# Performance work log

Hardware: AMD Instinct MI355X
Metric: run time of the kernel (lower is better)

Reference implementation:

```python
import math
import jax, jax.numpy as jnp
import numpy as np

N_NODES = 100000
N_EDGES = 3200000
D = 128
H = 8
DK = D // H


def setup_inputs() -> dict:
    key = jax.random.key(0)
    ks = jax.random.split(key, 12)
    s = 1.0 / math.sqrt(D)
    return {
        "feat": jax.random.normal(ks[0], (N_NODES, D), jnp.float32),
        "Wk": jax.random.normal(ks[1], (D, D), jnp.float32) * s,
        "bk": jax.random.normal(ks[2], (D,), jnp.float32) * s,
        "Wq": jax.random.normal(ks[3], (D, D), jnp.float32) * s,
        "bq": jax.random.normal(ks[4], (D,), jnp.float32) * s,
        "Wv": jax.random.normal(ks[5], (D, D), jnp.float32) * s,
        "bv": jax.random.normal(ks[6], (D,), jnp.float32) * s,
        "w_att": jax.random.normal(ks[7], (H, DK, DK), jnp.float32) * (1.0 / math.sqrt(DK)),
        "w_msg": jax.random.normal(ks[8], (H, DK, DK), jnp.float32) * (1.0 / math.sqrt(DK)),
        "mu": jax.random.uniform(ks[9], (1,), jnp.float32, 0.5, 1.5),
        "src": jax.random.randint(ks[10], (N_EDGES,), 0, N_NODES, jnp.int32),
        "dst": jax.random.randint(ks[11], (N_EDGES,), 0, N_NODES, jnp.int32),
    }


def reference(feat, Wk, bk, Wq, bq, Wv, bv, w_att, w_msg, mu, src, dst):
    N = feat.shape[0]
    # node projections, per-head relation transforms
    k = (feat @ Wk.T + bk).reshape(N, H, DK)            # (N,H,dk)
    v = (feat @ Wv.T + bv).reshape(N, H, DK)
    q = (feat @ Wq.T + bq).reshape(N, H, DK)
    k = jnp.einsum('nhi,hij->nhj', k, w_att)
    v = jnp.einsum('nhi,hij->nhj', v, w_msg)
    # edge-wise q (dst) . k (src) attention logits
    logits = jnp.einsum('ehd,ehd->eh', q[dst], k[src])  # (E,H)
    logits = logits * (mu[0] / math.sqrt(DK))
    # segment softmax over incoming edges of each dst node
    m = jax.ops.segment_max(logits, dst, num_segments=N)   # (N,H)
    ex = jnp.exp(logits - m[dst])
    denom = jax.ops.segment_sum(ex, dst, num_segments=N)   # (N,H)
    attn = ex / denom[dst]                                  # (E,H)
    # weighted message aggregation
    msg = v[src] * attn[..., None]                          # (E,H,dk)
    h = jax.ops.segment_sum(msg, dst, num_segments=N)       # (N,H,dk)
    return h.reshape(N, H * DK)
```

## Files before the change

kernel.cpp:

```cpp
#include <hip/hip_runtime.h>
#include <hip/hip_bf16.h>
#include <hip/hip_fp16.h>
#include <stdint.h>

#define DD 128
#define HH 8
#define DKK 16

#define BSHIFT 7
#define BNODES (1 << BSHIFT)
#define SC_EPT 16

typedef __attribute__((ext_vector_type(8))) short bf16x8;
typedef __attribute__((ext_vector_type(4))) float f32x4;
typedef _Float16 h2 __attribute__((ext_vector_type(2)));
union u32h2 { unsigned u; h2 h; };

__device__ __forceinline__ float bfhi2f(unsigned u) {
  union { unsigned i; float f; } c; c.i = u & 0xFFFF0000u; return c.f;
}
__device__ __forceinline__ float bflo2f(unsigned u) {
  union { unsigned i; float f; } c; c.i = u << 16; return c.f;
}
__device__ __forceinline__ unsigned short f2bf(float f) {
  __hip_bfloat16 b = __float2bfloat16(f);
  return *reinterpret_cast<unsigned short*>(&b);
}

__global__ __launch_bounds__(256) void prep_weights(
    const float* __restrict__ Wq, const float* __restrict__ bq,
    const float* __restrict__ Wk, const float* __restrict__ bk,
    const float* __restrict__ Wv, const float* __restrict__ bv,
    const float* __restrict__ w_att, const float* __restrict__ w_msg,
    const float* __restrict__ mu,
    unsigned short* __restrict__ WcatT, float* __restrict__ bcat) {
  int gid = blockIdx.x * blockDim.x + threadIdx.x;
  if (gid >= DD * 384) return;
  int f = gid / 384;
  int o = gid % 384;
  float scale = mu[0] * 0.25f;
  float w;
  if (o < 128) {
    w = Wq[o * DD + f] * scale;
  } else if (o < 256) {
    int c = o - 128, h = c >> 4, j = c & 15;
    float s = 0.f;
#pragma unroll
    for (int i = 0; i < 16; ++i)
      s += Wk[(h * 16 + i) * DD + f] * w_att[h * 256 + i * 16 + j];
    w = s;
  } else {
    int c = o - 256, h = c >> 4, j = c & 15;
    float s = 0.f;
#pragma unroll
    for (int i = 0; i < 16; ++i)
      s += Wv[(h * 16 + i) * DD + f] * w_msg[h * 256 + i * 16 + j];
    w = s;
  }
  WcatT[(size_t)o * DD + f] = f2bf(w);
  if (f == 0) {
    float b;
    if (o < 128) {
      b = bq[o] * scale;
    } else if (o < 256) {
      int c = o - 128, h = c >> 4, j = c & 15;
      float s = 0.f;
#pragma unroll
      for (int i = 0; i < 16; ++i)
        s += bk[h * 16 + i] * w_att[h * 256 + i * 16 + j];
      b = s;
    } else {
      int c = o - 256, h = c >> 4, j = c & 15;
      float s = 0.f;
#pragma unroll
      for (int i = 0; i < 16; ++i)
        s += bv[h * 16 + i] * w_msg[h * 256 + i * 16 + j];
      b = s;
    }
    bcat[o] = b;
  }
}

__global__ __launch_bounds__(256) void proj_gemm(
    const float* __restrict__ feat, const unsigned short* __restrict__ WcatT,
    const float* __restrict__ bcat, float* __restrict__ Q,
    unsigned char* __restrict__ KVrow, unsigned short* __restrict__ S,
    int N) {
  int row0 = blockIdx.x * 128;
  int wave = threadIdx.x >> 6, lane = threadIdx.x & 63;
  int lrow = lane & 15, lk = lane >> 4;

  bf16x8 a0[4], a1[4];
#pragma unroll
  for (int fr = 0; fr < 2; ++fr) {
    int arow = row0 + wave * 32 + fr * 16 + lrow;
    const float* ap = feat + (size_t)(arow < N ? arow : 0) * DD;
#pragma unroll
    for (int ks = 0; ks < 4; ++ks) {
      float4 v0 = *(const float4*)(ap + ks * 32 + lk * 8);
      float4 v1 = *(const float4*)(ap + ks * 32 + lk * 8 + 4);
      union { bf16x8 v; unsigned short s[8]; } u;
      u.s[0] = f2bf(v0.x); u.s[1] = f2bf(v0.y);
      u.s[2] = f2bf(v0.z); u.s[3] = f2bf(v0.w);
      u.s[4] = f2bf(v1.x); u.s[5] = f2bf(v1.y);
      u.s[6] = f2bf(v1.z); u.s[7] = f2bf(v1.w);
      if (fr == 0) a0[ks] = u.v; else a1[ks] = u.v;
    }
  }

#pragma unroll
  for (int nf = 0; nf < 24; ++nf) {
    f32x4 acc0 = (f32x4){0.f, 0.f, 0.f, 0.f};
    f32x4 acc1 = (f32x4){0.f, 0.f, 0.f, 0.f};
#pragma unroll
    for (int ks = 0; ks < 4; ++ks) {
      bf16x8 b = *(const bf16x8*)(WcatT + (size_t)(nf * 16 + lrow) * DD +
                                  ks * 32 + lk * 8);
      acc0 = __builtin_amdgcn_mfma_f32_16x16x32_bf16(a0[ks], b, acc0, 0, 0, 0);
      acc1 = __builtin_amdgcn_mfma_f32_16x16x32_bf16(a1[ks], b, acc1, 0, 0, 0);
    }
    int col = nf * 16 + lrow;
    float bias = bcat[col];
#pragma unroll
    for (int fr = 0; fr < 2; ++fr) {
      f32x4 acc = fr == 0 ? acc0 : acc1;
      int outrow = row0 + wave * 32 + fr * 16 + lk * 4;
#pragma unroll
      for (int r = 0; r < 4; ++r) {
        int grow = outrow + r;
        float c = acc[r] + bias;
        if (nf < 8) {
          if (grow < N) Q[(size_t)grow * DD + col] = c;
        } else if (nf < 16) {
          int h = nf - 8;
          if (grow < N)
            *(__half*)(KVrow + (size_t)grow * 384 + h * 48 + lrow * 2) =
                __float2half(c);
        } else {
          int h = nf - 16;
          float av = fabsf(c);
          av = fmaxf(av, __shfl_xor(av, 1));
          av = fmaxf(av, __shfl_xor(av, 2));
          av = fmaxf(av, __shfl_xor(av, 4));
          av = fmaxf(av, __shfl_xor(av, 8));
          float iv = (av > 0.f) ? 127.f / av : 0.f;
          int qv = (int)rintf(c * iv) + 128;
          qv = qv < 0 ? 0 : (qv > 255 ? 255 : qv);
          unsigned tmp = (unsigned)qv << ((lrow & 3) * 8);
          tmp |= __shfl_xor(tmp, 1);
          tmp |= __shfl_xor(tmp, 2);
          if ((lrow & 3) == 0 && grow < N)
            *(unsigned*)(KVrow + (size_t)grow * 384 + h * 48 + 32 +
                         (lrow >> 2) * 4) = tmp;
          if (lrow == 0 && grow < N)
            S[(size_t)grow * 8 + h] = f2bf(av / 127.f);
        }
      }
    }
  }
}

__global__ __launch_bounds__(256) void bucket_hist(
    const int* __restrict__ dst, int* __restrict__ bucket_count, int E,
    int NB) {
  __shared__ int h[1024];
  int tid = threadIdx.x;
  for (int i = tid; i < NB; i += 256) h[i] = 0;
  __syncthreads();
  for (int e = blockIdx.x * blockDim.x + tid; e < E;
       e += gridDim.x * blockDim.x)
    atomicAdd(&h[dst[e] >> BSHIFT], 1);
  __syncthreads();
  for (int i = tid; i < NB; i += 256)
    if (h[i]) atomicAdd(&bucket_count[i], h[i]);
}

__global__ __launch_bounds__(64) void bucket_scan(
    const int* __restrict__ bucket_count, int* __restrict__ bucket_base,
    int* __restrict__ bucket_cursor, int NB) {
  int lane = threadIdx.x;
  int running = 0;
  for (int c0 = 0; c0 < NB; c0 += 64) {
    int idx = c0 + lane;
    int v = (idx < NB) ? bucket_count[idx] : 0;
    int s = v;
#pragma unroll
    for (int off = 1; off < 64; off <<= 1) {
      int t = __shfl_up(s, off);
      if (lane >= off) s += t;
    }
    int excl = running + s - v;
    if (idx < NB) {
      bucket_base[idx] = excl;
      bucket_cursor[idx] = excl;
    }
    running += __shfl(s, 63);
  }
}

__global__ __launch_bounds__(256) void bucket_scatter(
    const int* __restrict__ src, const int* __restrict__ dst,
    int* __restrict__ bucket_cursor, unsigned* __restrict__ ebuf, int E,
    int NB) {
  __shared__ int h[1024];
  __shared__ int cur[1024];
  int tid = threadIdx.x;
  int base0 = blockIdx.x * (256 * SC_EPT);
  for (int i = tid; i < NB; i += 256) h[i] = 0;
  __syncthreads();
  int myd[SC_EPT], mys[SC_EPT];
#pragma unroll
  for (int i = 0; i < SC_EPT; ++i) {
    int e = base0 + i * 256 + tid;
    if (e < E) {
      myd[i] = dst[e];
      mys[i] = src[e];
      atomicAdd(&h[myd[i] >> BSHIFT], 1);
    } else {
      myd[i] = -1;
    }
  }
  __syncthreads();
  for (int i = tid; i < NB; i += 256)
    cur[i] = h[i] ? atomicAdd(&bucket_cursor[i], h[i]) : 0;
  __syncthreads();
#pragma unroll
  for (int i = 0; i < SC_EPT; ++i) {
    if (myd[i] >= 0) {
      int b = myd[i] >> BSHIFT;
      int p = atomicAdd(&cur[b], 1);
      ebuf[p] = ((unsigned)(myd[i] & (BNODES - 1)) << 17) | (unsigned)mys[i];
    }
  }
}

__global__ __launch_bounds__(256) void bucket_to_csr(
    const unsigned* __restrict__ ebuf, const int* __restrict__ bucket_base,
    const int* __restrict__ bucket_count, int* __restrict__ rowptr,
    int* __restrict__ deg, int* __restrict__ esrc, int N) {
  __shared__ int h[BNODES];
  __shared__ int sc[BNODES];
  __shared__ int cur[BNODES];
  int b = blockIdx.x;
  int tid = threadIdx.x;
  int start = bucket_base[b];
  int cnt = bucket_count[b];
  if (tid < BNODES) h[tid] = 0;
  __syncthreads();
  for (int i = tid; i < cnt; i += 256)
    atomicAdd(&h[ebuf[start + i] >> 17], 1);
  __syncthreads();
  if (tid < BNODES) sc[tid] = h[tid];
  __syncthreads();
  for (int off = 1; off < BNODES; off <<= 1) {
    int t = 0;
    if (tid < BNODES && tid >= off) t = sc[tid - off];
    __syncthreads();
    if (tid < BNODES) sc[tid] += t;
    __syncthreads();
  }
  if (tid < BNODES) {
    int excl = sc[tid] - h[tid];
    int node = b * BNODES + tid;
    if (node < N) {
      rowptr[node] = start + excl;
      deg[node] = h[tid];
    }
    cur[tid] = excl;
  }
  __syncthreads();
  for (int i = tid; i < cnt; i += 256) {
    unsigned u = ebuf[start + i];
    int p = atomicAdd(&cur[u >> 17], 1);
    esrc[start + p] = (int)(u & 0x1FFFFu);
  }
}

__global__ __launch_bounds__(256) void node_aggregate(
    const int* __restrict__ esrc, const int* __restrict__ rowptr,
    const int* __restrict__ deg, const float* __restrict__ Q,
    const unsigned char* __restrict__ KVrow,
    const unsigned short* __restrict__ S,
    float* __restrict__ out, int N) {
  int n = blockIdx.x * 4 + (threadIdx.x >> 6);
  if (n >= N) return;
  int lane = threadIdx.x & 63;
  int h = lane & 7;
  int p = lane >> 3;

  h2 qh[8];
#pragma unroll
  for (int i = 0; i < 4; ++i) {
    float4 t = *(const float4*)(Q + (size_t)n * DD + h * DKK + i * 4);
    qh[i * 2 + 0] = (h2){(_Float16)t.x, (_Float16)t.y};
    qh[i * 2 + 1] = (h2){(_Float16)t.z, (_Float16)t.w};
  }
  int row = rowptr[n];
  int dg = deg[n];

  float acc[16];
#pragma unroll
  for (int j = 0; j < 16; ++j) acc[j] = 0.f;
  float den = 0.f, evsum = 0.f;

  for (int base = 0; base < dg; base += 64) {
    int myid = (base + lane < dg) ? esrc[row + base + lane] : 0;
    int cnt = min(64, dg - base);
    int iters = (cnt + 7) >> 3;
#pragma unroll 2
    for (int i = 0; i < iters; ++i) {
      int slot = i * 8 + p;
      int s = __shfl(myid, slot);
      float m = (base + slot < dg) ? 1.f : 0.f;
      const unsigned char* rp = KVrow + (size_t)s * 384 + h * 48;
      uint4 k0 = *(const uint4*)rp;
      uint4 k1 = *(const uint4*)(rp + 16);
      uint4 vq = *(const uint4*)(rp + 32);
      float sV = bflo2f((unsigned)S[(size_t)s * 8 + h]);
      u32h2 c0, c1, c2, c3;
      c0.u = k0.x; c1.u = k0.y; c2.u = k0.z; c3.u = k0.w;
      float dA = __builtin_amdgcn_fdot2(qh[0], c0.h, 0.f, false);
      float dB = __builtin_amdgcn_fdot2(qh[1], c1.h, 0.f, false);
      dA = __builtin_amdgcn_fdot2(qh[2], c2.h, dA, false);
      dB = __builtin_amdgcn_fdot2(qh[3], c3.h, dB, false);
      c0.u = k1.x; c1.u = k1.y; c2.u = k1.z; c3.u = k1.w;
      dA = __builtin_amdgcn_fdot2(qh[4], c0.h, dA, false);
      dB = __builtin_amdgcn_fdot2(qh[5], c1.h, dB, false);
      dA = __builtin_amdgcn_fdot2(qh[6], c2.h, dA, false);
      dB = __builtin_amdgcn_fdot2(qh[7], c3.h, dB, false);
      float dot = dA + dB;
      float ex = m * __expf(fminf(dot, 80.f));
      den += ex;
      float evs = ex * sV;
      evsum += evs;
      acc[0] = fmaf(evs, (float)(vq.x & 255), acc[0]);
      acc[1] = fmaf(evs, (float)((vq.x >> 8) & 255), acc[1]);
      acc[2] = fmaf(evs, (float)((vq.x >> 16) & 255), acc[2]);
      acc[3] = fmaf(evs, (float)(vq.x >> 24), acc[3]);
      acc[4] = fmaf(evs, (float)(vq.y & 255), acc[4]);
      acc[5] = fmaf(evs, (float)((vq.y >> 8) & 255), acc[5]);
      acc[6] = fmaf(evs, (float)((vq.y >> 16) & 255), acc[6]);
      acc[7] = fmaf(evs, (float)(vq.y >> 24), acc[7]);
      acc[8] = fmaf(evs, (float)(vq.z & 255), acc[8]);
      acc[9] = fmaf(evs, (float)((vq.z >> 8) & 255), acc[9]);
      acc[10] = fmaf(evs, (float)((vq.z >> 16) & 255), acc[10]);
      acc[11] = fmaf(evs, (float)(vq.z >> 24), acc[11]);
      acc[12] = fmaf(evs, (float)(vq.w & 255), acc[12]);
      acc[13] = fmaf(evs, (float)((vq.w >> 8) & 255), acc[13]);
      acc[14] = fmaf(evs, (float)((vq.w >> 16) & 255), acc[14]);
      acc[15] = fmaf(evs, (float)(vq.w >> 24), acc[15]);
    }
  }

#pragma unroll
  for (int j = 0; j < 16; ++j) {
    acc[j] += __shfl_xor(acc[j], 8);
    acc[j] += __shfl_xor(acc[j], 16);
    acc[j] += __shfl_xor(acc[j], 32);
  }
  den += __shfl_xor(den, 8);
  den += __shfl_xor(den, 16);
  den += __shfl_xor(den, 32);
  evsum += __shfl_xor(evsum, 8);
  evsum += __shfl_xor(evsum, 16);
  evsum += __shfl_xor(evsum, 32);

  if (p == 0) {
    float inv = (dg > 0 && den > 0.f) ? 1.0f / den : 0.f;
    float corr = 128.f * evsum;
#pragma unroll
    for (int i = 0; i < 4; ++i) {
      float4 o = make_float4((acc[i * 4 + 0] - corr) * inv,
                             (acc[i * 4 + 1] - corr) * inv,
                             (acc[i * 4 + 2] - corr) * inv,
                             (acc[i * 4 + 3] - corr) * inv);
      *(float4*)(out + (size_t)n * DD + h * DKK + i * 4) = o;
    }
  }
}

extern "C" void kernel_launch(void* const* d_in, const int* in_sizes, int n_in,
                              void* d_out, int out_size, void* d_ws,
                              size_t ws_size, hipStream_t stream) {
  const float* feat = (const float*)d_in[0];
  const float* Wk = (const float*)d_in[1];
  const float* bk = (const float*)d_in[2];
  const float* Wq = (const float*)d_in[3];
  const float* bq = (const float*)d_in[4];
  const float* Wv = (const float*)d_in[5];
  const float* bv = (const float*)d_in[6];
  const float* w_att = (const float*)d_in[7];
  const float* w_msg = (const float*)d_in[8];
  const float* mu = (const float*)d_in[9];
  const int* src = (const int*)d_in[10];
  const int* dst = (const int*)d_in[11];

  int N = in_sizes[0] / DD;
  int E = in_sizes[10];
  int NB = (N + BNODES - 1) >> BSHIFT;

  char* ws = (char*)d_ws;
  unsigned short* WcatT = (unsigned short*)ws; ws += (size_t)DD * 384 * 2;
  float* bcat = (float*)ws; ws += 384 * 4;
  ws = (char*)(((uintptr_t)ws + 255) & ~(uintptr_t)255);
  float* Q = (float*)ws; ws += (size_t)N * DD * 4;
  unsigned char* KVrow = (unsigned char*)ws; ws += (size_t)N * 384;
  ws = (char*)(((uintptr_t)ws + 255) & ~(uintptr_t)255);
  unsigned short* S = (unsigned short*)ws; ws += (size_t)N * HH * 2;
  ws = (char*)(((uintptr_t)ws + 255) & ~(uintptr_t)255);
  int* deg = (int*)ws; ws += (size_t)N * 4;
  int* rowptr = (int*)ws; ws += (size_t)N * 4;
  int* bucket_count = (int*)ws; ws += 1024 * 4;
  int* bucket_base = (int*)ws; ws += 1024 * 4;
  int* bucket_cursor = (int*)ws; ws += 1024 * 4;
  ws = (char*)(((uintptr_t)ws + 255) & ~(uintptr_t)255);
  unsigned* ebuf = (unsigned*)ws; ws += (size_t)E * 4;
  int* esrc = (int*)ws; ws += (size_t)E * 4;

  hipMemsetAsync(bucket_count, 0, 1024 * 4, stream);

  prep_weights<<<(DD * 384 + 255) / 256, 256, 0, stream>>>(
      Wq, bq, Wk, bk, Wv, bv, w_att, w_msg, mu, WcatT, bcat);

  proj_gemm<<<(N + 127) / 128, 256, 0, stream>>>(feat, WcatT, bcat, Q, KVrow,
                                                 S, N);

  bucket_hist<<<256, 256, 0, stream>>>(dst, bucket_count, E, NB);
  bucket_scan<<<1, 64, 0, stream>>>(bucket_count, bucket_base, bucket_cursor,
                                    NB);
  int sc_blocks = (E + 256 * SC_EPT - 1) / (256 * SC_EPT);
  bucket_scatter<<<sc_blocks, 256, 0, stream>>>(src, dst, bucket_cursor, ebuf,
                                                E, NB);
  bucket_to_csr<<<NB, 256, 0, stream>>>(ebuf, bucket_base, bucket_count,
                                        rowptr, deg, esrc, N);

  node_aggregate<<<(N + 3) / 4, 256, 0, stream>>>(esrc, rowptr, deg, Q, KVrow,
                                                  S, (float*)d_out, N);
}
```

Baseline: 387.6 us.

## Merge independent kernels into horizontally fused launches and unroll aggregation loop

Combines weight prep with the dst histogram in one launch, and the projection GEMM with the bucket scatter in another, interleaving the two block roles by block index parity. This removes two kernel launches and lets the compute-bound GEMM overlap with the memory- and atomic-bound scatter on the GPU. It also raises the unroll factor of the per-edge aggregation loop from 2 to 4 for more memory-level parallelism. The cost is higher register and shared-memory pressure in the fused kernels, which may lower occupancy, plus some idle blocks when the two halves are unequal in size.

```diff
diff --git a/kernel.cpp b/kernel.cpp
--- a/kernel.cpp
+++ b/kernel.cpp
@@ -27,152 +27,73 @@
   return *reinterpret_cast<unsigned short*>(&b);
 }
 
-__global__ __launch_bounds__(256) void prep_weights(
+__global__ __launch_bounds__(256) void prep_and_hist(
     const float* __restrict__ Wq, const float* __restrict__ bq,
     const float* __restrict__ Wk, const float* __restrict__ bk,
     const float* __restrict__ Wv, const float* __restrict__ bv,
     const float* __restrict__ w_att, const float* __restrict__ w_msg,
     const float* __restrict__ mu,
-    unsigned short* __restrict__ WcatT, float* __restrict__ bcat) {
-  int gid = blockIdx.x * blockDim.x + threadIdx.x;
-  if (gid >= DD * 384) return;
-  int f = gid / 384;
-  int o = gid % 384;
-  float scale = mu[0] * 0.25f;
-  float w;
-  if (o < 128) {
-    w = Wq[o * DD + f] * scale;
-  } else if (o < 256) {
-    int c = o - 128, h = c >> 4, j = c & 15;
-    float s = 0.f;
-#pragma unroll
-    for (int i = 0; i < 16; ++i)
-      s += Wk[(h * 16 + i) * DD + f] * w_att[h * 256 + i * 16 + j];
-    w = s;
-  } else {
-    int c = o - 256, h = c >> 4, j = c & 15;
-    float s = 0.f;
-#pragma unroll
-    for (int i = 0; i < 16; ++i)
-      s += Wv[(h * 16 + i) * DD + f] * w_msg[h * 256 + i * 16 + j];
-    w = s;
-  }
-  WcatT[(size_t)o * DD + f] = f2bf(w);
-  if (f == 0) {
-    float b;
+    unsigned short* __restrict__ WcatT, float* __restrict__ bcat,
+    const int* __restrict__ dst, int* __restrict__ bucket_count, int E,
+    int NB) {
+  __shared__ int hst[1024];
+  int tid = threadIdx.x;
+  if (blockIdx.x < 192) {
+    int gid = blockIdx.x * 256 + tid;
+    if (gid >= DD * 384) return;
+    int f = gid / 384;
+    int o = gid % 384;
+    float scale = mu[0] * 0.25f;
+    float w;
     if (o < 128) {
-      b = bq[o] * scale;
+      w = Wq[o * DD + f] * scale;
     } else if (o < 256) {
       int c = o - 128, h = c >> 4, j = c & 15;
       float s = 0.f;
 #pragma unroll
       for (int i = 0; i < 16; ++i)
-        s += bk[h * 16 + i] * w_att[h * 256 + i * 16 + j];
-      b = s;
+        s += Wk[(h * 16 + i) * DD + f] * w_att[h * 256 + i * 16 + j];
+      w = s;
     } else {
       int c = o - 256, h = c >> 4, j = c & 15;
       float s = 0.f;
 #pragma unroll
       for (int i = 0; i < 16; ++i)
-        s += bv[h * 16 + i] * w_msg[h * 256 + i * 16 + j];
-      b = s;
-    }
-    bcat[o] = b;
-  }
-}
-
-__global__ __launch_bounds__(256) void proj_gemm(
-    const float* __restrict__ feat, const unsigned short* __restrict__ WcatT,
-    const float* __restrict__ bcat, float* __restrict__ Q,
-    unsigned char* __restrict__ KVrow, unsigned short* __restrict__ S,
-    int N) {
-  int row0 = blockIdx.x * 128;
-  int wave = threadIdx.x >> 6, lane = threadIdx.x & 63;
-  int lrow = lane & 15, lk = lane >> 4;
-
-  bf16x8 a0[4], a1[4];
-#pragma unroll
-  for (int fr = 0; fr < 2; ++fr) {
-    int arow = row0 + wave * 32 + fr * 16 + lrow;
-    const float* ap = feat + (size_t)(arow < N ? arow : 0) * DD;
-#pragma unroll
-    for (int ks = 0; ks < 4; ++ks) {
-      float4 v0 = *(const float4*)(ap + ks * 32 + lk * 8);
-      float4 v1 = *(const float4*)(ap + ks * 32 + lk * 8 + 4);
-      union { bf16x8 v; unsigned short s[8]; } u;
-      u.s[0] = f2bf(v0.x); u.s[1] = f2bf(v0.y);
-      u.s[2] = f2bf(v0.z); u.s[3] = f2bf(v0.w);
-      u.s[4] = f2bf(v1.x); u.s[5] = f2bf(v1.y);
-      u.s[6] = f2bf(v1.z); u.s[7] = f2bf(v1.w);
-      if (fr == 0) a0[ks] = u.v; else a1[ks] = u.v;
-    }
-  }
-
-#pragma unroll
-  for (int nf = 0; nf < 24; ++nf) {
-    f32x4 acc0 = (f32x4){0.f, 0.f, 0.f, 0.f};
-    f32x4 acc1 = (f32x4){0.f, 0.f, 0.f, 0.f};
-#pragma unroll
-    for (int ks = 0; ks < 4; ++ks) {
-      bf16x8 b = *(const bf16x8*)(WcatT + (size_t)(nf * 16 + lrow) * DD +
-                                  ks * 32 + lk * 8);
-      acc0 = __builtin_amdgcn_mfma_f32_16x16x32_bf16(a0[ks], b, acc0, 0, 0, 0);
-      acc1 = __builtin_amdgcn_mfma_f32_16x16x32_bf16(a1[ks], b, acc1, 0, 0, 0);
-    }
-    int col = nf * 16 + lrow;
-    float bias = bcat[col];
-#pragma unroll
-    for (int fr = 0; fr < 2; ++fr) {
-      f32x4 acc = fr == 0 ? acc0 : acc1;
-      int outrow = row0 + wave * 32 + fr * 16 + lk * 4;
-#pragma unroll
-      for (int r = 0; r < 4; ++r) {
-        int grow = outrow + r;
-        float c = acc[r] + bias;
-        if (nf < 8) {
-          if (grow < N) Q[(size_t)grow * DD + col] = c;
-        } else if (nf < 16) {
-          int h = nf - 8;
-          if (grow < N)
-            *(__half*)(KVrow + (size_t)grow * 384 + h * 48 + lrow * 2) =
-                __float2half(c);
-        } else {
-          int h = nf - 16;
-          float av = fabsf(c);
-          av = fmaxf(av, __shfl_xor(av, 1));
-          av = fmaxf(av, __shfl_xor(av, 2));
-          av = fmaxf(av, __shfl_xor(av, 4));
-          av = fmaxf(av, __shfl_xor(av, 8));
-          float iv = (av > 0.f) ? 127.f / av : 0.f;
-          int qv = (int)rintf(c * iv) + 128;
-          qv = qv < 0 ? 0 : (qv > 255 ? 255 : qv);
-          unsigned tmp = (unsigned)qv << ((lrow & 3) * 8);
-          tmp |= __shfl_xor(tmp, 1);
-          tmp |= __shfl_xor(tmp, 2);
-          if ((lrow & 3) == 0 && grow < N)
-            *(unsigned*)(KVrow + (size_t)grow * 384 + h * 48 + 32 +
-                         (lrow >> 2) * 4) = tmp;
-          if (lrow == 0 && grow < N)
-            S[(size_t)grow * 8 + h] = f2bf(av / 127.f);
-        }
-      }
-    }
-  }
-}
-
-__global__ __launch_bounds__(256) void bucket_hist(
-    const int* __restrict__ dst, int* __restrict__ bucket_count, int E,
-    int NB) {
-  __shared__ int h[1024];
-  int tid = threadIdx.x;
-  for (int i = tid; i < NB; i += 256) h[i] = 0;
-  __syncthreads();
-  for (int e = blockIdx.x * blockDim.x + tid; e < E;
-       e += gridDim.x * blockDim.x)
-    atomicAdd(&h[dst[e] >> BSHIFT], 1);
-  __syncthreads();
-  for (int i = tid; i < NB; i += 256)
-    if (h[i]) atomicAdd(&bucket_count[i], h[i]);
+        s += Wv[(h * 16 + i) * DD + f] * w_msg[h * 256 + i * 16 + j];
+      w = s;
+    }
+    WcatT[(size_t)o * DD + f] = f2bf(w);
+    if (f == 0) {
+      float b;
+      if (o < 128) {
+        b = bq[o] * scale;
+      } else if (o < 256) {
+        int c = o - 128, h = c >> 4, j = c & 15;
+        float s = 0.f;
+#pragma unroll
+        for (int i = 0; i < 16; ++i)
+          s += bk[h * 16 + i] * w_att[h * 256 + i * 16 + j];
+        b = s;
+      } else {
+        int c = o - 256, h = c >> 4, j = c & 15;
+        float s = 0.f;
+#pragma unroll
+        for (int i = 0; i < 16; ++i)
+          s += bv[h * 16 + i] * w_msg[h * 256 + i * 16 + j];
+        b = s;
+      }
+      bcat[o] = b;
+    }
+  } else {
+    int bi = blockIdx.x - 192;
+    for (int i = tid; i < NB; i += 256) hst[i] = 0;
+    __syncthreads();
+    for (int e = bi * 256 + tid; e < E; e += 256 * 256)
+      atomicAdd(&hst[dst[e] >> BSHIFT], 1);
+    __syncthreads();
+    for (int i = tid; i < NB; i += 256)
+      if (hst[i]) atomicAdd(&bucket_count[i], hst[i]);
+  }
 }
 
 __global__ __launch_bounds__(64) void bucket_scan(
@@ -198,38 +119,120 @@
   }
 }
 
-__global__ __launch_bounds__(256) void bucket_scatter(
+__global__ __launch_bounds__(256) void proj_and_scatter(
+    const float* __restrict__ feat, const unsigned short* __restrict__ WcatT,
+    const float* __restrict__ bcat, float* __restrict__ Q,
+    unsigned char* __restrict__ KVrow, unsigned short* __restrict__ S, int N,
     const int* __restrict__ src, const int* __restrict__ dst,
     int* __restrict__ bucket_cursor, unsigned* __restrict__ ebuf, int E,
-    int NB) {
-  __shared__ int h[1024];
+    int NB, int PB, int SB) {
+  __shared__ int hst[1024];
   __shared__ int cur[1024];
+  int sub = blockIdx.x >> 1;
   int tid = threadIdx.x;
-  int base0 = blockIdx.x * (256 * SC_EPT);
-  for (int i = tid; i < NB; i += 256) h[i] = 0;
-  __syncthreads();
-  int myd[SC_EPT], mys[SC_EPT];
-#pragma unroll
-  for (int i = 0; i < SC_EPT; ++i) {
-    int e = base0 + i * 256 + tid;
-    if (e < E) {
-      myd[i] = dst[e];
-      mys[i] = src[e];
-      atomicAdd(&h[myd[i] >> BSHIFT], 1);
-    } else {
-      myd[i] = -1;
-    }
-  }
-  __syncthreads();
-  for (int i = tid; i < NB; i += 256)
-    cur[i] = h[i] ? atomicAdd(&bucket_cursor[i], h[i]) : 0;
-  __syncthreads();
-#pragma unroll
-  for (int i = 0; i < SC_EPT; ++i) {
-    if (myd[i] >= 0) {
-      int b = myd[i] >> BSHIFT;
-      int p = atomicAdd(&cur[b], 1);
-      ebuf[p] = ((unsigned)(myd[i] & (BNODES - 1)) << 17) | (unsigned)mys[i];
+
+  if ((blockIdx.x & 1) == 0) {
+    if (sub >= PB) return;
+    int row0 = sub * 128;
+    int wave = tid >> 6, lane = tid & 63;
+    int lrow = lane & 15, lk = lane >> 4;
+
+    bf16x8 a0[4], a1[4];
+#pragma unroll
+    for (int fr = 0; fr < 2; ++fr) {
+      int arow = row0 + wave * 32 + fr * 16 + lrow;
+      const float* ap = feat + (size_t)(arow < N ? arow : 0) * DD;
+#pragma unroll
+      for (int ks = 0; ks < 4; ++ks) {
+        float4 v0 = *(const float4*)(ap + ks * 32 + lk * 8);
+        float4 v1 = *(const float4*)(ap + ks * 32 + lk * 8 + 4);
+        union { bf16x8 v; unsigned short s[8]; } u;
+        u.s[0] = f2bf(v0.x); u.s[1] = f2bf(v0.y);
+        u.s[2] = f2bf(v0.z); u.s[3] = f2bf(v0.w);
+        u.s[4] = f2bf(v1.x); u.s[5] = f2bf(v1.y);
+        u.s[6] = f2bf(v1.z); u.s[7] = f2bf(v1.w);
+        if (fr == 0) a0[ks] = u.v; else a1[ks] = u.v;
+      }
+    }
+
+#pragma unroll
+    for (int nf = 0; nf < 24; ++nf) {
+      f32x4 acc0 = (f32x4){0.f, 0.f, 0.f, 0.f};
+      f32x4 acc1 = (f32x4){0.f, 0.f, 0.f, 0.f};
+#pragma unroll
+      for (int ks = 0; ks < 4; ++ks) {
+        bf16x8 b = *(const bf16x8*)(WcatT + (size_t)(nf * 16 + lrow) * DD +
+                                    ks * 32 + lk * 8);
+        acc0 = __builtin_amdgcn_mfma_f32_16x16x32_bf16(a0[ks], b, acc0, 0, 0, 0);
+        acc1 = __builtin_amdgcn_mfma_f32_16x16x32_bf16(a1[ks], b, acc1, 0, 0, 0);
+      }
+      int col = nf * 16 + lrow;
+      float bias = bcat[col];
+#pragma unroll
+      for (int fr = 0; fr < 2; ++fr) {
+        f32x4 acc = fr == 0 ? acc0 : acc1;
+        int outrow = row0 + wave * 32 + fr * 16 + lk * 4;
+#pragma unroll
+        for (int r = 0; r < 4; ++r) {
+          int grow = outrow + r;
+          float c = acc[r] + bias;
+          if (nf < 8) {
+            if (grow < N) Q[(size_t)grow * DD + col] = c;
+          } else if (nf < 16) {
+            int h = nf - 8;
+            if (grow < N)
+              *(__half*)(KVrow + (size_t)grow * 384 + h * 48 + lrow * 2) =
+                  __float2half(c);
+          } else {
+            int h = nf - 16;
+            float av = fabsf(c);
+            av = fmaxf(av, __shfl_xor(av, 1));
+            av = fmaxf(av, __shfl_xor(av, 2));
+            av = fmaxf(av, __shfl_xor(av, 4));
+            av = fmaxf(av, __shfl_xor(av, 8));
+            float iv = (av > 0.f) ? 127.f / av : 0.f;
+            int qv = (int)rintf(c * iv) + 128;
+            qv = qv < 0 ? 0 : (qv > 255 ? 255 : qv);
+            unsigned tmp = (unsigned)qv << ((lrow & 3) * 8);
+            tmp |= __shfl_xor(tmp, 1);
+            tmp |= __shfl_xor(tmp, 2);
+            if ((lrow & 3) == 0 && grow < N)
+              *(unsigned*)(KVrow + (size_t)grow * 384 + h * 48 + 32 +
+                           (lrow >> 2) * 4) = tmp;
+            if (lrow == 0 && grow < N)
+              S[(size_t)grow * 8 + h] = f2bf(av / 127.f);
+          }
+        }
+      }
+    }
+  } else {
+    if (sub >= SB) return;
+    int base0 = sub * (256 * SC_EPT);
+    for (int i = tid; i < NB; i += 256) hst[i] = 0;
+    __syncthreads();
+    int myd[SC_EPT], mys[SC_EPT];
+#pragma unroll
+    for (int i = 0; i < SC_EPT; ++i) {
+      int e = base0 + i * 256 + tid;
+      if (e < E) {
+        myd[i] = dst[e];
+        mys[i] = src[e];
+        atomicAdd(&hst[myd[i] >> BSHIFT], 1);
+      } else {
+        myd[i] = -1;
+      }
+    }
+    __syncthreads();
+    for (int i = tid; i < NB; i += 256)
+      cur[i] = hst[i] ? atomicAdd(&bucket_cursor[i], hst[i]) : 0;
+    __syncthreads();
+#pragma unroll
+    for (int i = 0; i < SC_EPT; ++i) {
+      if (myd[i] >= 0) {
+        int b = myd[i] >> BSHIFT;
+        int p = atomicAdd(&cur[b], 1);
+        ebuf[p] = ((unsigned)(myd[i] & (BNODES - 1)) << 17) | (unsigned)mys[i];
+      }
     }
   }
 }
@@ -307,7 +310,7 @@
     int myid = (base + lane < dg) ? esrc[row + base + lane] : 0;
     int cnt = min(64, dg - base);
     int iters = (cnt + 7) >> 3;
-#pragma unroll 2
+#pragma unroll 4
     for (int i = 0; i < iters; ++i) {
       int slot = i * 8 + p;
       int s = __shfl(myid, slot);
@@ -419,18 +422,20 @@
 
   hipMemsetAsync(bucket_count, 0, 1024 * 4, stream);
 
-  prep_weights<<<(DD * 384 + 255) / 256, 256, 0, stream>>>(
-      Wq, bq, Wk, bk, Wv, bv, w_att, w_msg, mu, WcatT, bcat);
-
-  proj_gemm<<<(N + 127) / 128, 256, 0, stream>>>(feat, WcatT, bcat, Q, KVrow,
-                                                 S, N);
-
-  bucket_hist<<<256, 256, 0, stream>>>(dst, bucket_count, E, NB);
+  prep_and_hist<<<448, 256, 0, stream>>>(Wq, bq, Wk, bk, Wv, bv, w_att, w_msg,
+                                         mu, WcatT, bcat, dst, bucket_count, E,
+                                         NB);
+
   bucket_scan<<<1, 64, 0, stream>>>(bucket_count, bucket_base, bucket_cursor,
                                     NB);
-  int sc_blocks = (E + 256 * SC_EPT - 1) / (256 * SC_EPT);
-  bucket_scatter<<<sc_blocks, 256, 0, stream>>>(src, dst, bucket_cursor, ebuf,
-                                                E, NB);
+
+  int PB = (N + 127) / 128;
+  int SB = (E + 256 * SC_EPT - 1) / (256 * SC_EPT);
+  int MB = PB > SB ? PB : SB;
+  proj_and_scatter<<<2 * MB, 256, 0, stream>>>(
+      feat, WcatT, bcat, Q, KVrow, S, N, src, dst, bucket_cursor, ebuf, E, NB,
+      PB, SB);
+
   bucket_to_csr<<<NB, 256, 0, stream>>>(ebuf, bucket_base, bucket_count,
                                         rowptr, deg, esrc, N);
 
```

New measurement: 378.6 us. 2.3% less time.
